# Kernel tuning notes

Measured on AMD Instinct MI355X. Metric: run time of the kernel, lower is better.

## Reference

```python
import jax, jax.numpy as jnp
import numpy as np

H_SVD_MEDIUM_20 = np.array([+0.3279, +1.0, -0.9373, -0.8584, +0.6153, -0.5127, -0.3207, +0.8355,
                            -0.7528, +0.6792, +0.5284, -0.8558, -0.4101, -0.7967, -0.6088, -0.5275,
                            -0.2591, +0.894, +0.0663, +0.1645], dtype=np.float32)

def _inv_softplus(y, eps=1e-8):
    y = float(max(y, eps))
    return float(np.log(np.expm1(y)))

def setup_inputs() -> dict:
    key = jax.random.key(0)
    k1, k2, k3 = jax.random.split(key, 3)
    B, L, K, NUM_AA = 32, 8192, 64, 20
    seq = jax.random.randint(k1, (B, L), 0, NUM_AA, dtype=jnp.int64 if jax.config.jax_enable_x64 else jnp.int32)
    r = jax.random.uniform(k2, (B, L, K), dtype=jnp.float32) * 15.0
    j_idx = jax.random.randint(k3, (B, L, K), 0, L, dtype=seq.dtype)
    h = jnp.asarray(H_SVD_MEDIUM_20)                      # learned pair vector, SVD init
    r_half_raw = jnp.float32(_inv_softplus(6.5))
    tau_hp_raw = jnp.float32(_inv_softplus(1.5))
    return {"seq": seq, "r": r, "j_idx": j_idx, "h": h,
            "r_half_raw": r_half_raw, "tau_hp_raw": tau_hp_raw, "max_dist": 10}

def reference(seq, r, j_idx, h, r_half_raw, tau_hp_raw, max_dist):
    B, L, K = r.shape
    md = jnp.float32(max_dist)
    r_peak = jax.nn.softplus(r_half_raw)
    sigma = jax.nn.softplus(tau_hp_raw) + 0.1
    valid = (r < md - 1e-4).astype(r.dtype)               # [B,L,K]
    h_i = h[seq]                                          # [B,L]
    j_safe = jnp.clip(j_idx, 0, L - 1)
    seq_j = jnp.take_along_axis(seq, j_safe.reshape(B, L * K), axis=1).reshape(B, L, K)
    h_j = h[seq_j]                                        # [B,L,K]
    r_c = jnp.minimum(r, md)
    g = jnp.exp(-(r_c - r_peak) ** 2 / (2.0 * sigma ** 2)) * valid
    E_hp_i = jnp.sum(h_i[..., None] * h_j * g, axis=-1)   # [B,L]
    return E_hp_i
```

## Files before the change

### kernel.cpp

```cpp
#include <hip/hip_runtime.h>


#define BB 32
#define LL 8192
#define KK 64
#define TPB 512
#define RPB 512
#define NWAVE 8
#define NCHUNK 16

__device__ __forceinline__ void dma16(const void* g, void* l) {
    __builtin_amdgcn_global_load_lds(
        (const __attribute__((address_space(1))) void*)g,
        (__attribute__((address_space(3))) void*)l, 16, 0, 0);
}

__device__ __forceinline__ float row16_sum(float x) {
    x += __int_as_float(__builtin_amdgcn_mov_dpp(__float_as_int(x), 0x111, 0xF, 0xF, true));
    x += __int_as_float(__builtin_amdgcn_mov_dpp(__float_as_int(x), 0x112, 0xF, 0xF, true));
    x += __int_as_float(__builtin_amdgcn_mov_dpp(__float_as_int(x), 0x114, 0xF, 0xF, true));
    x += __int_as_float(__builtin_amdgcn_mov_dpp(__float_as_int(x), 0x118, 0xF, 0xF, true));
    return x;
}

__global__ __launch_bounds__(TPB) void _HydrophobicPairs_58256936403302_kernel(
    const int*   __restrict__ seq,
    const float* __restrict__ r,
    const int*   __restrict__ j_idx,
    const float* __restrict__ h,
    const float* __restrict__ r_half_raw,
    const float* __restrict__ tau_hp_raw,
    const int*   __restrict__ max_dist,
    float*       __restrict__ out)
{
    __shared__ float h_row[LL];
    __shared__ __align__(16) char sbuf[NWAVE][2][2048];

    const int tid  = threadIdx.x;
    const int wave = tid >> 6;
    const int lane = tid & 63;
    const int b     = blockIdx.x >> 4;
    const int lbase = (blockIdx.x & 15) * RPB;

    const int4* seq4 = (const int4*)(seq + b * LL);
    #pragma unroll
    for (int i = 0; i < 4; ++i) {
        const int e4 = i * TPB + tid;
        const int4 s = seq4[e4];
        ((float4*)h_row)[e4] = make_float4(h[s.x], h[s.y], h[s.z], h[s.w]);
    }

    const float md     = (float)max_dist[0];
    const float r_peak = log1pf(expf(r_half_raw[0]));
    const float sigma  = log1pf(expf(tau_hp_raw[0])) + 0.1f;
    const float nscale = -1.44269504f / (2.0f * sigma * sigma);
    const float c1     = -2.0f * nscale * r_peak;
    const float c0     = nscale * r_peak * r_peak;
    const float vthr   = md - 1e-4f;

    __syncthreads();

    const int l0 = lbase + wave * 64;
    const char* rg = (const char*)(r     + (long)(b * LL + l0) * KK) + lane * 16;
    const char* jg = (const char*)(j_idx + (long)(b * LL + l0) * KK) + lane * 16;

    dma16(rg + 0 * 1024, &sbuf[wave][0][0]);
    dma16(jg + 0 * 1024, &sbuf[wave][0][1024]);
    dma16(rg + 1 * 1024, &sbuf[wave][1][0]);
    dma16(jg + 1 * 1024, &sbuf[wave][1][1024]);

    const int myrow = lane >> 4;
    const int klane = lane & 15;

    #pragma unroll
    for (int c = 0; c < NCHUNK; ++c) {
        if      (c == 0)          asm volatile("s_waitcnt vmcnt(2)" ::: "memory");
        else if (c == 1)          asm volatile("s_waitcnt vmcnt(3)" ::: "memory");
        else if (c == NCHUNK - 1) asm volatile("s_waitcnt vmcnt(2)" ::: "memory");
        else                      asm volatile("s_waitcnt vmcnt(4)" ::: "memory");

        const int slot = c & 1;
        const float4 rc = *(const float4*)(&sbuf[wave][slot][lane * 16]);
        const int4   jc = *(const int4*)(&sbuf[wave][slot][1024 + lane * 16]);
        asm volatile("s_waitcnt lgkmcnt(0)" ::: "memory");

        if (c + 2 < NCHUNK) {
            dma16(rg + (c + 2) * 1024, &sbuf[wave][slot][0]);
            dma16(jg + (c + 2) * 1024, &sbuf[wave][slot][1024]);
        }

        float acc = 0.0f;
        #pragma unroll
        for (int u = 0; u < 4; ++u) {
            const float rv = (&rc.x)[u];
            const unsigned j = (unsigned)(&jc.x)[u] & (LL - 1);
            const float hj = h_row[j];
            const float uexp = fmaf(rv, fmaf(nscale, rv, c1), c0);
            float g = exp2f(uexp);
            g = (rv < vthr) ? g : 0.0f;
            acc = fmaf(hj, g, acc);
        }

        acc = row16_sum(acc);

        if (klane == 15) {
            const int lrow = l0 + c * 4 + myrow;
            out[b * LL + lrow] = h_row[lrow] * acc;
        }
    }
}

extern "C" void kernel_launch(void* const* d_in, const int* in_sizes, int n_in,
                              void* d_out, int out_size, void* d_ws, size_t ws_size,
                              hipStream_t stream) {
    const int*   seq        = (const int*)d_in[0];
    const float* r          = (const float*)d_in[1];
    const int*   j_idx      = (const int*)d_in[2];
    const float* h          = (const float*)d_in[3];
    const float* r_half_raw = (const float*)d_in[4];
    const float* tau_hp_raw = (const float*)d_in[5];
    const int*   max_dist   = (const int*)d_in[6];
    float*       out        = (float*)d_out;

    _HydrophobicPairs_58256936403302_kernel<<<dim3(BB * (LL / RPB)), dim3(TPB), 0, stream>>>(
        seq, r, j_idx, h, r_half_raw, tau_hp_raw, max_dist, out);
}
```

Before: 160.6 us.

## Replace LDS DMA double-buffering with deep register-prefetch pipeline of global loads

```diff
diff --git a/kernel.cpp b/kernel.cpp
--- a/kernel.cpp
+++ b/kernel.cpp
@@ -8,12 +8,10 @@
 #define RPB 512
 #define NWAVE 8
 #define NCHUNK 16
+#define DEPTH 6
 
-__device__ __forceinline__ void dma16(const void* g, void* l) {
-    __builtin_amdgcn_global_load_lds(
-        (const __attribute__((address_space(1))) void*)g,
-        (__attribute__((address_space(3))) void*)l, 16, 0, 0);
-}
+typedef float f32x4 __attribute__((ext_vector_type(4)));
+typedef int   i32x4 __attribute__((ext_vector_type(4)));
 
 __device__ __forceinline__ float row16_sum(float x) {
     x += __int_as_float(__builtin_amdgcn_mov_dpp(__float_as_int(x), 0x111, 0xF, 0xF, true));
@@ -23,7 +21,19 @@
     return x;
 }
 
-__global__ __launch_bounds__(TPB) void _HydrophobicPairs_58256936403302_kernel(
+#define ISSUE(c) do {                                                          \
+    asm volatile("global_load_dwordx4 %0, %1, off"                             \
+                 : "=v"(rs[c]) : "v"(rlane + (c) * 256));                      \
+    asm volatile("global_load_dwordx4 %0, %1, off"                             \
+                 : "=v"(js[c]) : "v"(jlane + (c) * 256));                      \
+} while (0)
+
+#define WAITV(n) do {                                                          \
+    asm volatile("s_waitcnt vmcnt(" #n ")" ::: "memory");                      \
+    __builtin_amdgcn_sched_barrier(0);                                         \
+} while (0)
+
+__global__ __launch_bounds__(TPB, 4) void _HydrophobicPairs_58256936403302_kernel(
     const int*   __restrict__ seq,
     const float* __restrict__ r,
     const int*   __restrict__ j_idx,
@@ -34,7 +44,7 @@
     float*       __restrict__ out)
 {
     __shared__ float h_row[LL];
-    __shared__ __align__(16) char sbuf[NWAVE][2][2048];
+    __shared__ float res[NWAVE][64];
 
     const int tid  = threadIdx.x;
     const int wave = tid >> 6;
@@ -61,39 +71,37 @@
     __syncthreads();
 
     const int l0 = lbase + wave * 64;
-    const char* rg = (const char*)(r     + (long)(b * LL + l0) * KK) + lane * 16;
-    const char* jg = (const char*)(j_idx + (long)(b * LL + l0) * KK) + lane * 16;
+    const float* rlane = r     + (size_t)(b * LL + l0) * KK + (lane << 2);
+    const int*   jlane = j_idx + (size_t)(b * LL + l0) * KK + (lane << 2);
 
-    dma16(rg + 0 * 1024, &sbuf[wave][0][0]);
-    dma16(jg + 0 * 1024, &sbuf[wave][0][1024]);
-    dma16(rg + 1 * 1024, &sbuf[wave][1][0]);
-    dma16(jg + 1 * 1024, &sbuf[wave][1][1024]);
+    f32x4 rs[NCHUNK];
+    i32x4 js[NCHUNK];
+
+    #pragma unroll
+    for (int p = 0; p < DEPTH; ++p) ISSUE(p);
 
     const int myrow = lane >> 4;
     const int klane = lane & 15;
 
     #pragma unroll
     for (int c = 0; c < NCHUNK; ++c) {
-        if      (c == 0)          asm volatile("s_waitcnt vmcnt(2)" ::: "memory");
-        else if (c == 1)          asm volatile("s_waitcnt vmcnt(3)" ::: "memory");
-        else if (c == NCHUNK - 1) asm volatile("s_waitcnt vmcnt(2)" ::: "memory");
-        else                      asm volatile("s_waitcnt vmcnt(4)" ::: "memory");
+        if      (c <= NCHUNK - DEPTH) WAITV(10);
+        else if (c == 11)             WAITV(8);
+        else if (c == 12)             WAITV(6);
+        else if (c == 13)             WAITV(4);
+        else if (c == 14)             WAITV(2);
+        else                          WAITV(0);
 
-        const int slot = c & 1;
-        const float4 rc = *(const float4*)(&sbuf[wave][slot][lane * 16]);
-        const int4   jc = *(const int4*)(&sbuf[wave][slot][1024 + lane * 16]);
-        asm volatile("s_waitcnt lgkmcnt(0)" ::: "memory");
+        if (c + DEPTH < NCHUNK) ISSUE(c + DEPTH);
 
-        if (c + 2 < NCHUNK) {
-            dma16(rg + (c + 2) * 1024, &sbuf[wave][slot][0]);
-            dma16(jg + (c + 2) * 1024, &sbuf[wave][slot][1024]);
-        }
+        const f32x4 rc = rs[c];
+        const i32x4 jc = js[c];
 
         float acc = 0.0f;
         #pragma unroll
         for (int u = 0; u < 4; ++u) {
-            const float rv = (&rc.x)[u];
-            const unsigned j = (unsigned)(&jc.x)[u] & (LL - 1);
+            const float rv = rc[u];
+            const unsigned j = (unsigned)jc[u] & (LL - 1);
             const float hj = h_row[j];
             const float uexp = fmaf(rv, fmaf(nscale, rv, c1), c0);
             float g = exp2f(uexp);
@@ -103,11 +111,11 @@
 
         acc = row16_sum(acc);
 
-        if (klane == 15) {
-            const int lrow = l0 + c * 4 + myrow;
-            out[b * LL + lrow] = h_row[lrow] * acc;
-        }
+        if (klane == 15) res[wave][(c << 2) | myrow] = acc;
     }
+
+    const int lrow = l0 + lane;
+    out[b * LL + lrow] = h_row[lrow] * res[wave][lane];
 }
 
 extern "C" void kernel_launch(void* const* d_in, const int* in_sizes, int n_in,
```

After: 157.6 us. About the same (-1.9%).

## Split waves between direct nontemporal loads and LDS DMA, coalesce output stores

Applied to the files above, without the earlier changes.

```diff
diff --git a/kernel.cpp b/kernel.cpp
--- a/kernel.cpp
+++ b/kernel.cpp
@@ -8,6 +8,9 @@
 #define RPB 512
 #define NWAVE 8
 #define NCHUNK 16
+
+typedef float f32x4 __attribute__((ext_vector_type(4)));
+typedef int   i32x4 __attribute__((ext_vector_type(4)));
 
 __device__ __forceinline__ void dma16(const void* g, void* l) {
     __builtin_amdgcn_global_load_lds(
@@ -23,7 +26,24 @@
     return x;
 }
 
-__global__ __launch_bounds__(TPB) void _HydrophobicPairs_58256936403302_kernel(
+__device__ __forceinline__ float chunk_acc(f32x4 rc, i32x4 jc, const float* h_row,
+                                           float nscale, float c1, float c0,
+                                           float vthr) {
+    float acc = 0.0f;
+    #pragma unroll
+    for (int u = 0; u < 4; ++u) {
+        const float rv = rc[u];
+        const unsigned j = (unsigned)jc[u] & (LL - 1);
+        const float hj = h_row[j];
+        const float uexp = fmaf(rv, fmaf(nscale, rv, c1), c0);
+        float g = exp2f(uexp);
+        g = (rv < vthr) ? g : 0.0f;
+        acc = fmaf(hj, g, acc);
+    }
+    return row16_sum(acc);
+}
+
+__global__ __launch_bounds__(TPB, 6) void _HydrophobicPairs_58256936403302_kernel(
     const int*   __restrict__ seq,
     const float* __restrict__ r,
     const int*   __restrict__ j_idx,
@@ -34,7 +54,8 @@
     float*       __restrict__ out)
 {
     __shared__ float h_row[LL];
-    __shared__ __align__(16) char sbuf[NWAVE][2][2048];
+    __shared__ float res[NWAVE][64];
+    __shared__ __align__(16) char sbuf[4][2][2048];
 
     const int tid  = threadIdx.x;
     const int wave = tid >> 6;
@@ -61,53 +82,53 @@
     __syncthreads();
 
     const int l0 = lbase + wave * 64;
-    const char* rg = (const char*)(r     + (long)(b * LL + l0) * KK) + lane * 16;
-    const char* jg = (const char*)(j_idx + (long)(b * LL + l0) * KK) + lane * 16;
-
-    dma16(rg + 0 * 1024, &sbuf[wave][0][0]);
-    dma16(jg + 0 * 1024, &sbuf[wave][0][1024]);
-    dma16(rg + 1 * 1024, &sbuf[wave][1][0]);
-    dma16(jg + 1 * 1024, &sbuf[wave][1][1024]);
-
     const int myrow = lane >> 4;
     const int klane = lane & 15;
 
-    #pragma unroll
-    for (int c = 0; c < NCHUNK; ++c) {
-        if      (c == 0)          asm volatile("s_waitcnt vmcnt(2)" ::: "memory");
-        else if (c == 1)          asm volatile("s_waitcnt vmcnt(3)" ::: "memory");
-        else if (c == NCHUNK - 1) asm volatile("s_waitcnt vmcnt(2)" ::: "memory");
-        else                      asm volatile("s_waitcnt vmcnt(4)" ::: "memory");
+    if (wave < 4) {
+        const f32x4* r4 = (const f32x4*)(r     + (size_t)(b * LL + l0) * KK) + lane;
+        const i32x4* j4 = (const i32x4*)(j_idx + (size_t)(b * LL + l0) * KK) + lane;
+        #pragma unroll
+        for (int c = 0; c < NCHUNK; ++c) {
+            const f32x4 rc = __builtin_nontemporal_load(r4 + c * 64);
+            const i32x4 jc = __builtin_nontemporal_load(j4 + c * 64);
+            const float acc = chunk_acc(rc, jc, h_row, nscale, c1, c0, vthr);
+            if (klane == 15) res[wave][(c << 2) | myrow] = acc;
+        }
+    } else {
+        const int dw = wave - 4;
+        const char* rg = (const char*)(r     + (size_t)(b * LL + l0) * KK) + lane * 16;
+        const char* jg = (const char*)(j_idx + (size_t)(b * LL + l0) * KK) + lane * 16;
 
-        const int slot = c & 1;
-        const float4 rc = *(const float4*)(&sbuf[wave][slot][lane * 16]);
-        const int4   jc = *(const int4*)(&sbuf[wave][slot][1024 + lane * 16]);
-        asm volatile("s_waitcnt lgkmcnt(0)" ::: "memory");
+        dma16(rg + 0 * 1024, &sbuf[dw][0][0]);
+        dma16(jg + 0 * 1024, &sbuf[dw][0][1024]);
+        dma16(rg + 1 * 1024, &sbuf[dw][1][0]);
+        dma16(jg + 1 * 1024, &sbuf[dw][1][1024]);
 
-        if (c + 2 < NCHUNK) {
-            dma16(rg + (c + 2) * 1024, &sbuf[wave][slot][0]);
-            dma16(jg + (c + 2) * 1024, &sbuf[wave][slot][1024]);
-        }
+        #pragma unroll
+        for (int c = 0; c < NCHUNK; ++c) {
+            if (c < NCHUNK - 1) asm volatile("s_waitcnt vmcnt(2)" ::: "memory");
+            else                asm volatile("s_waitcnt vmcnt(0)" ::: "memory");
+            __builtin_amdgcn_sched_barrier(0);
 
-        float acc = 0.0f;
-        #pragma unroll
-        for (int u = 0; u < 4; ++u) {
-            const float rv = (&rc.x)[u];
-            const unsigned j = (unsigned)(&jc.x)[u] & (LL - 1);
-            const float hj = h_row[j];
-            const float uexp = fmaf(rv, fmaf(nscale, rv, c1), c0);
-            float g = exp2f(uexp);
-            g = (rv < vthr) ? g : 0.0f;
-            acc = fmaf(hj, g, acc);
-        }
+            const int slot = c & 1;
+            const f32x4 rc = *(const f32x4*)(&sbuf[dw][slot][lane * 16]);
+            const i32x4 jc = *(const i32x4*)(&sbuf[dw][slot][1024 + lane * 16]);
+            asm volatile("s_waitcnt lgkmcnt(0)" ::: "memory");
+            __builtin_amdgcn_sched_barrier(0);
 
-        acc = row16_sum(acc);
+            if (c + 2 < NCHUNK) {
+                dma16(rg + (c + 2) * 1024, &sbuf[dw][slot][0]);
+                dma16(jg + (c + 2) * 1024, &sbuf[dw][slot][1024]);
+            }
 
-        if (klane == 15) {
-            const int lrow = l0 + c * 4 + myrow;
-            out[b * LL + lrow] = h_row[lrow] * acc;
+            const float acc = chunk_acc(rc, jc, h_row, nscale, c1, c0, vthr);
+            if (klane == 15) res[wave][(c << 2) | myrow] = acc;
         }
     }
+
+    const int lrow = l0 + lane;
+    out[b * LL + lrow] = h_row[lrow] * res[wave][lane];
 }
 
 extern "C" void kernel_launch(void* const* d_in, const int* in_sizes, int n_in,
```

Result: no change. 157.7 us (-1.8%).
